# Optimization experiments

Hardware: AMD Instinct MI355X
Metric: run time of the kernel (lower is better)

## Reference

```python
import jax, jax.numpy as jnp
import numpy as np

N = 50000      # nodes
E = 800000     # edges (before self-loops)
F_IN = 128     # node_feature_dim
H = 128        # hidden_dim
HEADS = 4
DH = H // HEADS
L = 3          # num_layers
OUT = 128      # output_dim
B = 64         # graphs in batch
EPS = 1e-5
NEG_SLOPE = 0.2


def layer_norm(x, g, b):
    mu = jnp.mean(x, axis=-1, keepdims=True)
    var = jnp.mean(jnp.square(x - mu), axis=-1, keepdims=True)
    return (x - mu) * jax.lax.rsqrt(var + EPS) * g + b


def setup_inputs() -> dict:
    key = jax.random.key(0)
    ks = jax.random.split(key, 10)
    s = 0.05
    x = jax.random.normal(ks[0], (N, F_IN), jnp.float32)
    edge_index = jax.random.randint(ks[1], (2, E), 0, N, dtype=jnp.int32)
    batch = jnp.sort(jax.random.randint(ks[2], (N,), 0, B, dtype=jnp.int32))
    return {
        "x": x,
        "edge_index": edge_index,
        "batch": batch,
        # node encoder: Linear + LayerNorm
        "W0": jax.random.normal(ks[3], (F_IN, H), jnp.float32) * s,
        "b0": jnp.zeros((H,), jnp.float32),
        "g0": jnp.ones((H,), jnp.float32),
        "be0": jnp.zeros((H,), jnp.float32),
        # GAT layers (stacked over L)
        "Wg": jax.random.normal(ks[4], (L, H, H), jnp.float32) * s,
        "att_src": jax.random.normal(ks[5], (L, HEADS, DH), jnp.float32) * s,
        "att_dst": jax.random.normal(ks[6], (L, HEADS, DH), jnp.float32) * s,
        "bg": jnp.zeros((L, H), jnp.float32),
        "gg": jnp.ones((L, H), jnp.float32),
        "bgg": jnp.zeros((L, H), jnp.float32),
        # output projection: Linear + LayerNorm
        "Wp": jax.random.normal(ks[7], (H, OUT), jnp.float32) * s,
        "bp": jnp.zeros((OUT,), jnp.float32),
        "gp": jnp.ones((OUT,), jnp.float32),
        "bep": jnp.zeros((OUT,), jnp.float32),
    }


def gnn_forward(x, src, dst, W0, b0, g0, be0, Wg, att_src, att_dst, bg, gg, bgg, Wp, bp, gp, bep, batch):
    n = x.shape[0]
    h = jax.nn.silu(layer_norm(x @ W0 + b0, g0, be0))  # [N, H]
    for l in range(L):
        identity = h
        hh = (h @ Wg[l]).reshape(n, HEADS, DH)                 # [N, heads, dh]
        a_s = jnp.einsum('nhd,hd->nh', hh, att_src[l])         # [N, heads]
        a_d = jnp.einsum('nhd,hd->nh', hh, att_dst[l])
        e = jax.nn.leaky_relu(a_s[src] + a_d[dst], NEG_SLOPE)  # [E', heads]
        m = jax.lax.stop_gradient(jax.ops.segment_max(e, dst, num_segments=n))
        alpha = jnp.exp(e - m[dst])
        denom = jax.ops.segment_sum(alpha, dst, num_segments=n)
        alpha = alpha / denom[dst]                             # segment softmax over dst
        msg = hh[src] * alpha[:, :, None]                      # [E', heads, dh]
        out = jax.ops.segment_sum(msg, dst, num_segments=n).reshape(n, H) + bg[l]
        h = jax.nn.silu(layer_norm(out, gg[l], bgg[l])) + identity
    # global mean pool per graph
    cnt = jax.ops.segment_sum(jnp.ones((n, 1), h.dtype), batch, num_segments=B)
    pooled = jax.ops.segment_sum(h, batch, num_segments=B) / jnp.maximum(cnt, 1.0)
    return jax.nn.silu(layer_norm(pooled @ Wp + bp, gp, bep))  # [B, OUT]


def reference(x, edge_index, batch, W0, b0, g0, be0, Wg, att_src, att_dst, bg, gg, bgg, Wp, bp, gp, bep):
    n = x.shape[0]
    loops = jnp.arange(n, dtype=edge_index.dtype)  # PyG GATConv add_self_loops=True
    src = jnp.concatenate([edge_index[0], loops])
    dst = jnp.concatenate([edge_index[1], loops])
    return gnn_forward(x, src, dst, W0, b0, g0, be0, Wg, att_src, att_dst, bg, gg, bgg, Wp, bp, gp, bep, batch)
```

## Files before the change

kernel.cpp:

```cpp
#include <hip/hip_runtime.h>

#define NN    50000
#define EE    800000
#define EPE   850000
#define NPAD  50048
#define BGR   64
#define MAXCH 128
#define NB    98
#define CHUNK 4096
#define NBLK  208
#define BCAP  12288

typedef __attribute__((ext_vector_type(8))) short bf16x8;
typedef __attribute__((ext_vector_type(4))) float f32x4;
typedef __attribute__((ext_vector_type(2))) float f32x2;

__device__ __forceinline__ float bf2f(unsigned short u) {
    return __uint_as_float(((unsigned)u) << 16);
}
__device__ __forceinline__ unsigned short f2bf(float f) {
    unsigned u = __float_as_uint(f);
    unsigned r = (u + 0x7FFFu + ((u >> 16) & 1u)) >> 16;
    return (unsigned short)r;
}
__device__ __forceinline__ float silu(float y) { return y / (1.f + __expf(-y)); }

__global__ void transpose_zero(const float* __restrict__ W0, const float* __restrict__ Wg,
                               unsigned short* __restrict__ WT, float* __restrict__ pooled) {
    __shared__ unsigned short tile[128][129];
    int b = blockIdx.x;
    if (b < 4) {
        const float* src = (b == 0) ? W0 : (Wg + (b - 1) * 16384);
        unsigned short* dst = WT + b * 16384;
        for (int i = threadIdx.x; i < 16384; i += 256) tile[i >> 7][i & 127] = f2bf(src[i]);
        __syncthreads();
        for (int i = threadIdx.x; i < 16384; i += 256) {
            int c = i >> 7, k = i & 127;
            dst[i] = tile[k][c];
        }
    } else {
        int j = (b - 4) * 256 + threadIdx.x;
        if (j < BGR * 128) pooled[j] = 0.f;
    }
}

__global__ __launch_bounds__(256) void bucket_hist(const int* __restrict__ eidx,
                                                   int* __restrict__ hist_blk) {
    __shared__ int lh[NB];
    for (int t = threadIdx.x; t < NB; t += 256) lh[t] = 0;
    __syncthreads();
    int base = blockIdx.x * CHUNK;
#pragma unroll
    for (int j = 0; j < CHUNK / 256; ++j) {
        int i = base + j * 256 + threadIdx.x;
        if (i < EPE) {
            int d = (i < EE) ? eidx[EE + i] : (i - EE);
            atomicAdd(&lh[d >> 9], 1);
        }
    }
    __syncthreads();
    for (int t = threadIdx.x; t < NB; t += 256)
        hist_blk[blockIdx.x * NB + t] = lh[t];
}

__global__ void scan_buckets(const int* __restrict__ hist_blk, int* __restrict__ blkOfs,
                             int* __restrict__ bucketBase) {
    __shared__ int tot[NB];
    __shared__ int base[NB];
    int t = threadIdx.x;
    if (t < NB) {
        int s = 0;
        for (int k = 0; k < NBLK; ++k) s += hist_blk[k * NB + t];
        tot[t] = s;
    }
    __syncthreads();
    if (t == 0) {
        int run = 0;
        for (int b = 0; b < NB; ++b) { base[b] = run; run += tot[b]; }
        bucketBase[NB] = EPE;
    }
    __syncthreads();
    if (t < NB) {
        int run = base[t];
        bucketBase[t] = run;
        for (int k = 0; k < NBLK; ++k) {
            blkOfs[k * NB + t] = run;
            run += hist_blk[k * NB + t];
        }
    }
}

__global__ __launch_bounds__(256) void bin_edges(const int* __restrict__ eidx,
                                                 const int* __restrict__ blkOfs,
                                                 unsigned* __restrict__ binned) {
    __shared__ unsigned staged[CHUNK];
    __shared__ int lhist[NB];
    __shared__ int lscan[NB];
    __shared__ int cnt2[NB];
    __shared__ int gofs[NB];
    int tid = threadIdx.x;
    for (int t = tid; t < NB; t += 256) { lhist[t] = 0; cnt2[t] = 0; }
    __syncthreads();
    int base = blockIdx.x * CHUNK;
    unsigned pk[CHUNK / 256];
#pragma unroll
    for (int j = 0; j < CHUNK / 256; ++j) {
        int i = base + j * 256 + tid;
        pk[j] = 0xFFFFFFFFu;
        if (i < EPE) {
            int s, d;
            if (i < EE) { s = eidx[i]; d = eidx[EE + i]; } else { s = i - EE; d = i - EE; }
            pk[j] = ((unsigned)s << 16) | (unsigned)d;
            atomicAdd(&lhist[d >> 9], 1);
        }
    }
    __syncthreads();
    if (tid == 0) {
        int run = 0;
        for (int b = 0; b < NB; ++b) { lscan[b] = run; run += lhist[b]; }
    }
    __syncthreads();
#pragma unroll
    for (int j = 0; j < CHUNK / 256; ++j) {
        if (pk[j] != 0xFFFFFFFFu) {
            int b = (int)((pk[j] & 0xFFFFu) >> 9);
            int lp = lscan[b] + atomicAdd(&cnt2[b], 1);
            staged[lp] = pk[j];
        }
    }
    for (int t = tid; t < NB; t += 256) gofs[t] = blkOfs[blockIdx.x * NB + t];
    __syncthreads();
    int nTot = lscan[NB - 1] + lhist[NB - 1];
    for (int i = tid; i < nTot; i += 256) {
        unsigned p = staged[i];
        int b = (int)((p & 0xFFFFu) >> 9);
        binned[gofs[b] + (i - lscan[b])] = p;
    }
}

__global__ __launch_bounds__(256) void build_csr(const unsigned* __restrict__ binned,
                                                 const int* __restrict__ bucketBase,
                                                 int* __restrict__ offs,
                                                 int* __restrict__ csr) {
    __shared__ int lcsr[BCAP];
    __shared__ int lcnt[512];
    __shared__ int lofs[512];
    __shared__ int lcur[512];
    __shared__ int psum[256];
    int b = blockIdx.x, tid = threadIdx.x;
    int n0 = b * 512;
    int o0 = bucketBase[b];
    int nTot = bucketBase[b + 1] - o0;
    if (nTot > BCAP) nTot = BCAP;
    for (int j = tid; j < 512; j += 256) lcnt[j] = 0;
    __syncthreads();
    for (int i = tid; i < nTot; i += 256)
        atomicAdd(&lcnt[binned[o0 + i] & 511u], 1);
    __syncthreads();
    int a0 = lcnt[2 * tid], a1 = lcnt[2 * tid + 1];
    psum[tid] = a0 + a1;
    __syncthreads();
    for (int d = 1; d < 256; d <<= 1) {
        int v = (tid >= d) ? psum[tid - d] : 0;
        __syncthreads(); psum[tid] += v; __syncthreads();
    }
    int exclPair = psum[tid] - (a0 + a1);
    lofs[2 * tid] = exclPair;
    lofs[2 * tid + 1] = exclPair + a0;
    lcur[2 * tid] = exclPair;
    lcur[2 * tid + 1] = exclPair + a0;
    __syncthreads();
    for (int j = tid; j < 512; j += 256) {
        int node = n0 + j;
        if (node < NN) offs[node] = o0 + lofs[j];
    }
    if (b == 0 && tid == 0) offs[NN] = EPE;
    for (int i = tid; i < nTot; i += 256) {
        unsigned p = binned[o0 + i];
        int pos = atomicAdd(&lcur[p & 511u], 1);
        if (pos < BCAP) lcsr[pos] = (int)(p >> 16);
    }
    __syncthreads();
    for (int i = tid; i < nTot; i += 256)
        csr[o0 + i] = lcsr[i];
}

__global__ __launch_bounds__(256) void gemm_encoder(
    const float* __restrict__ x, const unsigned short* __restrict__ WT,
    const float* __restrict__ b0, const float* __restrict__ g0,
    const float* __restrict__ be0, unsigned short* __restrict__ h) {
    int wave = threadIdx.x >> 6, lane = threadIdx.x & 63;
    int cl = lane & 15, q = lane >> 4;
    int row0 = blockIdx.x * 64 + wave * 16;
    int rA = row0 + cl; if (rA >= NN) rA = NN - 1;
    int kq = q * 8;
    f32x4 acc[8];
#pragma unroll
    for (int t = 0; t < 8; ++t) acc[t] = (f32x4){0.f, 0.f, 0.f, 0.f};
#pragma unroll
    for (int k0 = 0; k0 < 128; k0 += 32) {
        const float* xr = x + rA * 128 + k0 + kq;
        f32x4 f0 = *(const f32x4*)(xr);
        f32x4 f1 = *(const f32x4*)(xr + 4);
        bf16x8 a;
#pragma unroll
        for (int j = 0; j < 4; ++j) {
            a[j] = (short)f2bf(f0[j]);
            a[4 + j] = (short)f2bf(f1[j]);
        }
#pragma unroll
        for (int t = 0; t < 8; ++t) {
            bf16x8 b = *(const bf16x8*)(WT + (t * 16 + cl) * 128 + k0 + kq);
            acc[t] = __builtin_amdgcn_mfma_f32_16x16x32_bf16(a, b, acc[t], 0, 0, 0);
        }
    }
    float bcol[8], gcol[8], becol[8];
#pragma unroll
    for (int t = 0; t < 8; ++t) {
        int c = t * 16 + cl;
        bcol[t] = b0[c]; gcol[t] = g0[c]; becol[t] = be0[c];
    }
#pragma unroll
    for (int r = 0; r < 4; ++r) {
        int row = row0 + q * 4 + r;
        float v[8], s = 0.f, ss = 0.f;
#pragma unroll
        for (int t = 0; t < 8; ++t) {
            v[t] = acc[t][r] + bcol[t];
            s += v[t]; ss += v[t] * v[t];
        }
#pragma unroll
        for (int m = 1; m <= 8; m <<= 1) {
            s += __shfl_xor(s, m, 64); ss += __shfl_xor(ss, m, 64);
        }
        float mu = s * (1.f / 128.f);
        float var = ss * (1.f / 128.f) - mu * mu;
        float rstd = rsqrtf(var + 1e-5f);
        if (row < NN) {
#pragma unroll
            for (int t = 0; t < 8; ++t) {
                float y = (v[t] - mu) * rstd * gcol[t] + becol[t];
                h[row * 128 + t * 16 + cl] = f2bf(silu(y));
            }
        }
    }
}

__global__ __launch_bounds__(256) void gemm_gat(
    const unsigned short* __restrict__ h, const unsigned short* __restrict__ WT,
    const float* __restrict__ atts, const float* __restrict__ attd,
    unsigned char* __restrict__ hh8, float* __restrict__ a_s, float* __restrict__ a_d,
    float* __restrict__ es) {
    int wave = threadIdx.x >> 6, lane = threadIdx.x & 63;
    int cl = lane & 15, q = lane >> 4;
    int row0 = blockIdx.x * 64 + wave * 16;
    int rA = row0 + cl; if (rA >= NN) rA = NN - 1;
    int kq = q * 8;
    f32x4 acc[8];
#pragma unroll
    for (int t = 0; t < 8; ++t) acc[t] = (f32x4){0.f, 0.f, 0.f, 0.f};
#pragma unroll
    for (int k0 = 0; k0 < 128; k0 += 32) {
        bf16x8 a = *(const bf16x8*)(h + rA * 128 + k0 + kq);
#pragma unroll
        for (int t = 0; t < 8; ++t) {
            bf16x8 b = *(const bf16x8*)(WT + (t * 16 + cl) * 128 + k0 + kq);
            acc[t] = __builtin_amdgcn_mfma_f32_16x16x32_bf16(a, b, acc[t], 0, 0, 0);
        }
    }
#pragma unroll
    for (int r = 0; r < 4; ++r) {
        int row = row0 + q * 4 + r;
        if (row < NN) {
#pragma unroll
            for (int t = 0; t < 8; ++t) {
                unsigned pk = (unsigned)__builtin_amdgcn_cvt_pk_fp8_f32(acc[t][r], acc[t][r], 0, false);
                hh8[row * 128 + t * 16 + cl] = (unsigned char)(pk & 0xFFu);
            }
        }
    }
    float as_lo[4], as_hi[4], ad_lo[4], ad_hi[4];
#pragma unroll
    for (int hd = 0; hd < 4; ++hd) {
        as_lo[hd] = atts[hd * 32 + cl];      as_hi[hd] = atts[hd * 32 + 16 + cl];
        ad_lo[hd] = attd[hd * 32 + cl];      ad_hi[hd] = attd[hd * 32 + 16 + cl];
    }
#pragma unroll
    for (int r = 0; r < 4; ++r) {
        int row = row0 + q * 4 + r;
        float ps[4], pd[4];
#pragma unroll
        for (int hd = 0; hd < 4; ++hd) {
            float v0 = acc[2 * hd][r], v1 = acc[2 * hd + 1][r];
            ps[hd] = v0 * as_lo[hd] + v1 * as_hi[hd];
            pd[hd] = v0 * ad_lo[hd] + v1 * ad_hi[hd];
        }
#pragma unroll
        for (int m = 1; m <= 8; m <<= 1) {
#pragma unroll
            for (int hd = 0; hd < 4; ++hd) {
                ps[hd] += __shfl_xor(ps[hd], m, 64);
                pd[hd] += __shfl_xor(pd[hd], m, 64);
            }
        }
        if (row < NN && cl < 4) {
            float vs = (cl == 0) ? ps[0] : (cl == 1) ? ps[1] : (cl == 2) ? ps[2] : ps[3];
            float vd = (cl == 0) ? pd[0] : (cl == 1) ? pd[1] : (cl == 2) ? pd[2] : pd[3];
            a_s[row * 4 + cl] = vs;
            a_d[row * 4 + cl] = vd;
            float e = vs + vd;
            es[row * 4 + cl] = (e > 0.f) ? e : 0.2f * e;
        }
    }
}

__global__ __launch_bounds__(256) void gat_aggregate(
    const int* __restrict__ offs, const int* __restrict__ csr,
    const float* __restrict__ a_s, const float* __restrict__ a_d,
    const float* __restrict__ es, const unsigned char* __restrict__ hh8,
    unsigned short* __restrict__ h,
    const float* __restrict__ bg, const float* __restrict__ gg,
    const float* __restrict__ bgg) {
    __shared__ f32x4 lw[8][MAXCH];
    int wv = threadIdx.x >> 6;
    int lane = threadIdx.x & 63;
    int half = lane >> 5;
    int l32 = lane & 31;
    int ns = wv * 2 + half;
    int node = blockIdx.x * 8 + ns;
    int e0 = offs[node], e1 = offs[node + 1];
    int c0 = l32 * 4;
    int hd = l32 >> 3;
    f32x4 ad4 = *(const f32x4*)(a_d + node * 4);
    f32x4 e4  = *(const f32x4*)(es  + node * 4);
    float dacc[4];
    f32x4 xacc[4];
#pragma unroll
    for (int u = 0; u < 4; ++u) {
        dacc[u] = 0.f;
        xacc[u] = (f32x4){0.f, 0.f, 0.f, 0.f};
    }
    for (int base = e0; base < e1; base += MAXCH) {
        int cend = min(e1, base + MAXCH);
        for (int e = base + l32; e < cend; e += 32) {
            int s = csr[e];
            f32x4 as = *(const f32x4*)(a_s + s * 4);
            f32x4 o;
#pragma unroll
            for (int k = 0; k < 4; ++k) {
                float qq = as[k] + ad4[k];
                qq = (qq > 0.f) ? qq : 0.2f * qq;
                o[k] = __expf(qq - e4[k]);
            }
            lw[ns][e - base] = o;
        }
        asm volatile("s_waitcnt lgkmcnt(0)" ::: "memory");
        int n = cend - base;
        int j = 0;
        for (; j + 4 <= n; j += 4) {
            int s0 = csr[base + j], s1 = csr[base + j + 1];
            int s2 = csr[base + j + 2], s3 = csr[base + j + 3];
            float w0 = lw[ns][j + 0][hd];
            float w1 = lw[ns][j + 1][hd];
            float w2 = lw[ns][j + 2][hd];
            float w3 = lw[ns][j + 3][hd];
            unsigned v0 = *(const unsigned*)(hh8 + s0 * 128 + c0);
            unsigned v1 = *(const unsigned*)(hh8 + s1 * 128 + c0);
            unsigned v2 = *(const unsigned*)(hh8 + s2 * 128 + c0);
            unsigned v3 = *(const unsigned*)(hh8 + s3 * 128 + c0);
            f32x2 l0 = __builtin_amdgcn_cvt_pk_f32_fp8(v0, false);
            f32x2 h0 = __builtin_amdgcn_cvt_pk_f32_fp8(v0, true);
            f32x2 l1 = __builtin_amdgcn_cvt_pk_f32_fp8(v1, false);
            f32x2 h1 = __builtin_amdgcn_cvt_pk_f32_fp8(v1, true);
            f32x2 l2 = __builtin_amdgcn_cvt_pk_f32_fp8(v2, false);
            f32x2 h2 = __builtin_amdgcn_cvt_pk_f32_fp8(v2, true);
            f32x2 l3 = __builtin_amdgcn_cvt_pk_f32_fp8(v3, false);
            f32x2 h3 = __builtin_amdgcn_cvt_pk_f32_fp8(v3, true);
            dacc[0] += w0;
            xacc[0][0] += w0 * l0[0]; xacc[0][1] += w0 * l0[1];
            xacc[0][2] += w0 * h0[0]; xacc[0][3] += w0 * h0[1];
            dacc[1] += w1;
            xacc[1][0] += w1 * l1[0]; xacc[1][1] += w1 * l1[1];
            xacc[1][2] += w1 * h1[0]; xacc[1][3] += w1 * h1[1];
            dacc[2] += w2;
            xacc[2][0] += w2 * l2[0]; xacc[2][1] += w2 * l2[1];
            xacc[2][2] += w2 * h2[0]; xacc[2][3] += w2 * h2[1];
            dacc[3] += w3;
            xacc[3][0] += w3 * l3[0]; xacc[3][1] += w3 * l3[1];
            xacc[3][2] += w3 * h3[0]; xacc[3][3] += w3 * h3[1];
        }
        for (; j < n; ++j) {
            int s0 = csr[base + j];
            float w0 = lw[ns][j][hd];
            unsigned v0 = *(const unsigned*)(hh8 + s0 * 128 + c0);
            f32x2 l0 = __builtin_amdgcn_cvt_pk_f32_fp8(v0, false);
            f32x2 h0 = __builtin_amdgcn_cvt_pk_f32_fp8(v0, true);
            dacc[0] += w0;
            xacc[0][0] += w0 * l0[0]; xacc[0][1] += w0 * l0[1];
            xacc[0][2] += w0 * h0[0]; xacc[0][3] += w0 * h0[1];
        }
        if (cend < e1)
            asm volatile("s_waitcnt lgkmcnt(0)" ::: "memory");
    }
    float den = (dacc[0] + dacc[1]) + (dacc[2] + dacc[3]);
    f32x4 X;
#pragma unroll
    for (int k = 0; k < 4; ++k)
        X[k] = (xacc[0][k] + xacc[1][k]) + (xacc[2][k] + xacc[3][k]);
    float inv = 1.f / den;
    f32x4 bgv  = *(const f32x4*)(bg + c0);
    f32x4 ggv  = *(const f32x4*)(gg + c0);
    f32x4 bggv = *(const f32x4*)(bgg + c0);
    f32x4 o;
    float s = 0.f, ss = 0.f;
#pragma unroll
    for (int k = 0; k < 4; ++k) {
        o[k] = X[k] * inv + bgv[k];
        s += o[k]; ss += o[k] * o[k];
    }
#pragma unroll
    for (int m = 1; m <= 16; m <<= 1) {
        s += __shfl_xor(s, m, 64); ss += __shfl_xor(ss, m, 64);
    }
    float mu = s * (1.f / 128.f);
    float var = ss * (1.f / 128.f) - mu * mu;
    float rstd = rsqrtf(var + 1e-5f);
    uint2 idpk = *(const uint2*)(h + node * 128 + c0);
    float r0 = silu((o[0] - mu) * rstd * ggv[0] + bggv[0]) + bf2f((unsigned short)(idpk.x & 0xFFFFu));
    float r1 = silu((o[1] - mu) * rstd * ggv[1] + bggv[1]) + bf2f((unsigned short)(idpk.x >> 16));
    float r2 = silu((o[2] - mu) * rstd * ggv[2] + bggv[2]) + bf2f((unsigned short)(idpk.y & 0xFFFFu));
    float r3 = silu((o[3] - mu) * rstd * ggv[3] + bggv[3]) + bf2f((unsigned short)(idpk.y >> 16));
    uint2 pk;
    pk.x = (unsigned)f2bf(r0) | ((unsigned)f2bf(r1) << 16);
    pk.y = (unsigned)f2bf(r2) | ((unsigned)f2bf(r3) << 16);
    *(uint2*)(h + node * 128 + c0) = pk;
}

__global__ void pool_kernel(const unsigned short* __restrict__ h, const int* __restrict__ batch,
                            float* __restrict__ pooled) {
    int c = threadIdx.x;
    int r0 = blockIdx.x * 64;
    int rend = r0 + 64; if (rend > NN) rend = NN;
    int cur = batch[r0];
    float acc = 0.f;
    for (int r = r0; r < rend; ++r) {
        int b = batch[r];
        float v = bf2f(h[r * 128 + c]);
        if (b != cur) {
            atomicAdd(&pooled[cur * 128 + c], acc);
            acc = 0.f; cur = b;
        }
        acc += v;
    }
    atomicAdd(&pooled[cur * 128 + c], acc);
}

__global__ void final_kernel(const float* __restrict__ pooled, const int* __restrict__ batch,
                             const float* __restrict__ Wp, const float* __restrict__ bp,
                             const float* __restrict__ gp, const float* __restrict__ bep,
                             float* __restrict__ out) {
    __shared__ float p[128];
    __shared__ float red[128];
    __shared__ int bounds[2];
    int g = blockIdx.x, c = threadIdx.x;
    if (c == 0) {
        int lo = 0, hi = NN;
        while (lo < hi) { int m = (lo + hi) >> 1; if (batch[m] < g) lo = m + 1; else hi = m; }
        bounds[0] = lo;
        int lo2 = lo, hi2 = NN;
        while (lo2 < hi2) { int m = (lo2 + hi2) >> 1; if (batch[m] < g + 1) lo2 = m + 1; else hi2 = m; }
        bounds[1] = lo2;
    }
    __syncthreads();
    float cnt = (float)(bounds[1] - bounds[0]); if (cnt < 1.f) cnt = 1.f;
    p[c] = pooled[g * 128 + c] / cnt;
    __syncthreads();
    float acc = bp[c];
    for (int k = 0; k < 128; ++k) acc += p[k] * Wp[k * 128 + c];
    red[c] = acc;
    __syncthreads();
    if (c < 64) {
        float s = red[c] + red[c + 64];
#pragma unroll
        for (int m = 1; m <= 32; m <<= 1) s += __shfl_xor(s, m, 64);
        if (c == 0) red[0] = s;
    }
    __syncthreads();
    float mu = red[0] * (1.f / 128.f);
    __syncthreads();
    float dv = acc - mu;
    red[c] = dv * dv;
    __syncthreads();
    if (c < 64) {
        float s = red[c] + red[c + 64];
#pragma unroll
        for (int m = 1; m <= 32; m <<= 1) s += __shfl_xor(s, m, 64);
        if (c == 0) red[0] = s;
    }
    __syncthreads();
    float var = red[0] * (1.f / 128.f);
    float rstd = rsqrtf(var + 1e-5f);
    float y = dv * rstd * gp[c] + bep[c];
    out[g * 128 + c] = silu(y);
}

extern "C" void kernel_launch(void* const* d_in, const int* in_sizes, int n_in,
                              void* d_out, int out_size, void* d_ws, size_t ws_size,
                              hipStream_t stream) {
    const float* x    = (const float*)d_in[0];
    const int*   eidx = (const int*)d_in[1];
    const int*   batch= (const int*)d_in[2];
    const float* W0   = (const float*)d_in[3];
    const float* b0   = (const float*)d_in[4];
    const float* g0   = (const float*)d_in[5];
    const float* be0  = (const float*)d_in[6];
    const float* Wg   = (const float*)d_in[7];
    const float* atts = (const float*)d_in[8];
    const float* attd = (const float*)d_in[9];
    const float* bg   = (const float*)d_in[10];
    const float* gg   = (const float*)d_in[11];
    const float* bgg  = (const float*)d_in[12];
    const float* Wp   = (const float*)d_in[13];
    const float* bp   = (const float*)d_in[14];
    const float* gp   = (const float*)d_in[15];
    const float* bep  = (const float*)d_in[16];

    char* ws = (char*)d_ws;
    size_t off = 0;
    auto alloc = [&](size_t bytes) {
        void* p = ws + off;
        off = (off + bytes + 255) & ~(size_t)255;
        return p;
    };
    unsigned short* h        = (unsigned short*)alloc((size_t)NPAD * 128 * 2);
    unsigned char*  hh8      = (unsigned char*)alloc((size_t)NN * 128);
    float*          a_s      = (float*)alloc((size_t)NN * 4 * 4);
    float*          a_d      = (float*)alloc((size_t)NN * 4 * 4);
    float*          es       = (float*)alloc((size_t)NN * 4 * 4);
    int*            offs     = (int*)alloc((size_t)(NN + 1) * 4);
    int*            csr      = (int*)alloc((size_t)EPE * 4);
    unsigned*       binned   = (unsigned*)alloc((size_t)EPE * 4);
    int*            hist_blk = (int*)alloc((size_t)NBLK * NB * 4);
    int*            blkOfs   = (int*)alloc((size_t)NBLK * NB * 4);
    int*            bktBase  = (int*)alloc((size_t)(NB + 1) * 4);
    unsigned short* WT       = (unsigned short*)alloc(4 * 16384 * 2);
    float*          pooled   = (float*)alloc((size_t)BGR * 128 * 4);

    transpose_zero<<<4 + 32, 256, 0, stream>>>(W0, Wg, WT, pooled);
    bucket_hist<<<NBLK, 256, 0, stream>>>(eidx, hist_blk);
    scan_buckets<<<1, 128, 0, stream>>>(hist_blk, blkOfs, bktBase);
    bin_edges<<<NBLK, 256, 0, stream>>>(eidx, blkOfs, binned);
    build_csr<<<NB, 256, 0, stream>>>(binned, bktBase, offs, csr);

    gemm_encoder<<<NPAD / 64, 256, 0, stream>>>(x, WT, b0, g0, be0, h);
    for (int l = 0; l < 3; ++l) {
        gemm_gat<<<NPAD / 64, 256, 0, stream>>>(h, WT + (l + 1) * 16384,
                                                atts + l * 128, attd + l * 128,
                                                hh8, a_s, a_d, es);
        gat_aggregate<<<NN / 8, 256, 0, stream>>>(offs, csr, a_s, a_d, es, hh8, h,
                                                  bg + l * 128, gg + l * 128,
                                                  bgg + l * 128);
    }
    pool_kernel<<<(NN + 63) / 64, 128, 0, stream>>>(h, batch, pooled);
    final_kernel<<<BGR, 128, 0, stream>>>(pooled, batch, Wp, bp, gp, bep, (float*)d_out);
}
```

Measured before the change: 381.2 us.

## Fuse preprocessing kernels with encoder/GAT GEMMs and relayout fp8 features

Merges the weight transpose, pool zeroing and edge histogram into one launch. The bucket scan rides alongside the encoder GEMM, and edge binning rides alongside the first GAT GEMM, so independent CSR-building work runs concurrently with dense work and fewer kernels launch. The fp8 projected features are stored with a head-interleaved column layout. The aggregation kernel caches both source indices and all four head weights in shared memory, then accumulates per-column across heads, which removes repeated csr reads. This trades simpler, coalesced per-node epilogue writes for scalar bf16 stores and extra shuffles for the denominator.

```diff
diff --git a/kernel.cpp b/kernel.cpp
--- a/kernel.cpp
+++ b/kernel.cpp
@@ -5,11 +5,11 @@
 #define EPE   850000
 #define NPAD  50048
 #define BGR   64
-#define MAXCH 128
 #define NB    98
 #define CHUNK 4096
 #define NBLK  208
 #define BCAP  12288
+#define AGCH  64
 
 typedef __attribute__((ext_vector_type(8))) short bf16x8;
 typedef __attribute__((ext_vector_type(4))) float f32x4;
@@ -25,9 +25,14 @@
 }
 __device__ __forceinline__ float silu(float y) { return y / (1.f + __expf(-y)); }
 
-__global__ void transpose_zero(const float* __restrict__ W0, const float* __restrict__ Wg,
-                               unsigned short* __restrict__ WT, float* __restrict__ pooled) {
+__global__ __launch_bounds__(256) void pre_kernel(const float* __restrict__ W0,
+                                                  const float* __restrict__ Wg,
+                                                  unsigned short* __restrict__ WT,
+                                                  float* __restrict__ pooled,
+                                                  const int* __restrict__ eidx,
+                                                  int* __restrict__ hist_blk) {
     __shared__ unsigned short tile[128][129];
+    __shared__ int lh[NB];
     int b = blockIdx.x;
     if (b < 4) {
         const float* src = (b == 0) ? W0 : (Wg + (b - 1) * 16384);
@@ -38,70 +43,215 @@
             int c = i >> 7, k = i & 127;
             dst[i] = tile[k][c];
         }
+    } else if (b < 36) {
+        int j = (b - 4) * 256 + threadIdx.x;
+        pooled[j] = 0.f;
     } else {
-        int j = (b - 4) * 256 + threadIdx.x;
-        if (j < BGR * 128) pooled[j] = 0.f;
-    }
-}
-
-__global__ __launch_bounds__(256) void bucket_hist(const int* __restrict__ eidx,
-                                                   int* __restrict__ hist_blk) {
-    __shared__ int lh[NB];
-    for (int t = threadIdx.x; t < NB; t += 256) lh[t] = 0;
-    __syncthreads();
-    int base = blockIdx.x * CHUNK;
-#pragma unroll
-    for (int j = 0; j < CHUNK / 256; ++j) {
-        int i = base + j * 256 + threadIdx.x;
-        if (i < EPE) {
-            int d = (i < EE) ? eidx[EE + i] : (i - EE);
-            atomicAdd(&lh[d >> 9], 1);
-        }
-    }
-    __syncthreads();
-    for (int t = threadIdx.x; t < NB; t += 256)
-        hist_blk[blockIdx.x * NB + t] = lh[t];
-}
-
-__global__ void scan_buckets(const int* __restrict__ hist_blk, int* __restrict__ blkOfs,
-                             int* __restrict__ bucketBase) {
+        int cb = b - 36;
+        for (int t = threadIdx.x; t < NB; t += 256) lh[t] = 0;
+        __syncthreads();
+        int base = cb * CHUNK;
+#pragma unroll
+        for (int j = 0; j < CHUNK / 256; ++j) {
+            int i = base + j * 256 + threadIdx.x;
+            if (i < EPE) {
+                int d = (i < EE) ? eidx[EE + i] : (i - EE);
+                atomicAdd(&lh[d >> 9], 1);
+            }
+        }
+        __syncthreads();
+        for (int t = threadIdx.x; t < NB; t += 256)
+            hist_blk[cb * NB + t] = lh[t];
+    }
+}
+
+__global__ __launch_bounds__(256) void scan_encoder_kernel(
+    const int* __restrict__ hist_blk, int* __restrict__ blkOfs, int* __restrict__ bucketBase,
+    const float* __restrict__ x, const unsigned short* __restrict__ WT,
+    const float* __restrict__ b0, const float* __restrict__ g0,
+    const float* __restrict__ be0, unsigned short* __restrict__ h) {
     __shared__ int tot[NB];
-    __shared__ int base[NB];
-    int t = threadIdx.x;
-    if (t < NB) {
-        int s = 0;
-        for (int k = 0; k < NBLK; ++k) s += hist_blk[k * NB + t];
-        tot[t] = s;
-    }
-    __syncthreads();
-    if (t == 0) {
-        int run = 0;
-        for (int b = 0; b < NB; ++b) { base[b] = run; run += tot[b]; }
-        bucketBase[NB] = EPE;
-    }
-    __syncthreads();
-    if (t < NB) {
-        int run = base[t];
-        bucketBase[t] = run;
-        for (int k = 0; k < NBLK; ++k) {
-            blkOfs[k * NB + t] = run;
-            run += hist_blk[k * NB + t];
-        }
-    }
-}
-
-__global__ __launch_bounds__(256) void bin_edges(const int* __restrict__ eidx,
-                                                 const int* __restrict__ blkOfs,
-                                                 unsigned* __restrict__ binned) {
+    __shared__ int bas[NB];
+    if (blockIdx.x == 0) {
+        int t = threadIdx.x;
+        if (t < NB) {
+            int s = 0;
+            for (int k = 0; k < NBLK; ++k) s += hist_blk[k * NB + t];
+            tot[t] = s;
+        }
+        __syncthreads();
+        if (t == 0) {
+            int run = 0;
+            for (int b = 0; b < NB; ++b) { bas[b] = run; run += tot[b]; }
+            bucketBase[NB] = EPE;
+        }
+        __syncthreads();
+        if (t < NB) {
+            int run = bas[t];
+            bucketBase[t] = run;
+            for (int k = 0; k < NBLK; ++k) {
+                blkOfs[k * NB + t] = run;
+                run += hist_blk[k * NB + t];
+            }
+        }
+        return;
+    }
+    int bid = blockIdx.x - 1;
+    int wave = threadIdx.x >> 6, lane = threadIdx.x & 63;
+    int cl = lane & 15, q = lane >> 4;
+    int row0 = bid * 64 + wave * 16;
+    int rA = row0 + cl; if (rA >= NN) rA = NN - 1;
+    int kq = q * 8;
+    f32x4 acc[8];
+#pragma unroll
+    for (int t = 0; t < 8; ++t) acc[t] = (f32x4){0.f, 0.f, 0.f, 0.f};
+#pragma unroll
+    for (int k0 = 0; k0 < 128; k0 += 32) {
+        const float* xr = x + rA * 128 + k0 + kq;
+        f32x4 f0 = *(const f32x4*)(xr);
+        f32x4 f1 = *(const f32x4*)(xr + 4);
+        bf16x8 a;
+#pragma unroll
+        for (int j = 0; j < 4; ++j) {
+            a[j] = (short)f2bf(f0[j]);
+            a[4 + j] = (short)f2bf(f1[j]);
+        }
+#pragma unroll
+        for (int t = 0; t < 8; ++t) {
+            bf16x8 b = *(const bf16x8*)(WT + (t * 16 + cl) * 128 + k0 + kq);
+            acc[t] = __builtin_amdgcn_mfma_f32_16x16x32_bf16(a, b, acc[t], 0, 0, 0);
+        }
+    }
+    float bcol[8], gcol[8], becol[8];
+#pragma unroll
+    for (int t = 0; t < 8; ++t) {
+        int c = t * 16 + cl;
+        bcol[t] = b0[c]; gcol[t] = g0[c]; becol[t] = be0[c];
+    }
+#pragma unroll
+    for (int r = 0; r < 4; ++r) {
+        int row = row0 + q * 4 + r;
+        float v[8], s = 0.f, ss = 0.f;
+#pragma unroll
+        for (int t = 0; t < 8; ++t) {
+            v[t] = acc[t][r] + bcol[t];
+            s += v[t]; ss += v[t] * v[t];
+        }
+#pragma unroll
+        for (int m = 1; m <= 8; m <<= 1) {
+            s += __shfl_xor(s, m, 64); ss += __shfl_xor(ss, m, 64);
+        }
+        float mu = s * (1.f / 128.f);
+        float var = ss * (1.f / 128.f) - mu * mu;
+        float rstd = rsqrtf(var + 1e-5f);
+        if (row < NN) {
+#pragma unroll
+            for (int t = 0; t < 8; ++t) {
+                float y = (v[t] - mu) * rstd * gcol[t] + becol[t];
+                h[row * 128 + t * 16 + cl] = f2bf(silu(y));
+            }
+        }
+    }
+}
+
+__device__ __forceinline__ void gat_gemm_body(
+    int bid, const unsigned short* __restrict__ h, const unsigned short* __restrict__ WT,
+    const float* __restrict__ atts, const float* __restrict__ attd,
+    unsigned char* __restrict__ hh8, float* __restrict__ a_s, float* __restrict__ a_d,
+    float* __restrict__ es) {
+    int wave = threadIdx.x >> 6, lane = threadIdx.x & 63;
+    int cl = lane & 15, q = lane >> 4;
+    int row0 = bid * 64 + wave * 16;
+    int rA = row0 + cl; if (rA >= NN) rA = NN - 1;
+    int kq = q * 8;
+    f32x4 acc[8];
+#pragma unroll
+    for (int t = 0; t < 8; ++t) acc[t] = (f32x4){0.f, 0.f, 0.f, 0.f};
+#pragma unroll
+    for (int k0 = 0; k0 < 128; k0 += 32) {
+        bf16x8 a = *(const bf16x8*)(h + rA * 128 + k0 + kq);
+#pragma unroll
+        for (int t = 0; t < 8; ++t) {
+            bf16x8 b = *(const bf16x8*)(WT + (t * 16 + cl) * 128 + k0 + kq);
+            acc[t] = __builtin_amdgcn_mfma_f32_16x16x32_bf16(a, b, acc[t], 0, 0, 0);
+        }
+    }
+#pragma unroll
+    for (int r = 0; r < 4; ++r) {
+        int row = row0 + q * 4 + r;
+        if (row < NN) {
+#pragma unroll
+            for (int t = 0; t < 8; ++t) {
+                unsigned pk = (unsigned)__builtin_amdgcn_cvt_pk_fp8_f32(acc[t][r], acc[t][r], 0, false);
+                int c = t * 16 + cl;
+                hh8[row * 128 + ((c & 31) << 2) + (c >> 5)] = (unsigned char)(pk & 0xFFu);
+            }
+        }
+    }
+    float as_lo[4], as_hi[4], ad_lo[4], ad_hi[4];
+#pragma unroll
+    for (int hd = 0; hd < 4; ++hd) {
+        as_lo[hd] = atts[hd * 32 + cl];      as_hi[hd] = atts[hd * 32 + 16 + cl];
+        ad_lo[hd] = attd[hd * 32 + cl];      ad_hi[hd] = attd[hd * 32 + 16 + cl];
+    }
+#pragma unroll
+    for (int r = 0; r < 4; ++r) {
+        int row = row0 + q * 4 + r;
+        float ps[4], pd[4];
+#pragma unroll
+        for (int hd = 0; hd < 4; ++hd) {
+            float v0 = acc[2 * hd][r], v1 = acc[2 * hd + 1][r];
+            ps[hd] = v0 * as_lo[hd] + v1 * as_hi[hd];
+            pd[hd] = v0 * ad_lo[hd] + v1 * ad_hi[hd];
+        }
+#pragma unroll
+        for (int m = 1; m <= 8; m <<= 1) {
+#pragma unroll
+            for (int hd = 0; hd < 4; ++hd) {
+                ps[hd] += __shfl_xor(ps[hd], m, 64);
+                pd[hd] += __shfl_xor(pd[hd], m, 64);
+            }
+        }
+        if (row < NN && cl < 4) {
+            float vs = (cl == 0) ? ps[0] : (cl == 1) ? ps[1] : (cl == 2) ? ps[2] : ps[3];
+            float vd = (cl == 0) ? pd[0] : (cl == 1) ? pd[1] : (cl == 2) ? pd[2] : pd[3];
+            a_s[row * 4 + cl] = vs;
+            a_d[row * 4 + cl] = vd;
+            float e = vs + vd;
+            es[row * 4 + cl] = (e > 0.f) ? e : 0.2f * e;
+        }
+    }
+}
+
+__global__ __launch_bounds__(256) void gemm_gat(
+    const unsigned short* __restrict__ h, const unsigned short* __restrict__ WT,
+    const float* __restrict__ atts, const float* __restrict__ attd,
+    unsigned char* __restrict__ hh8, float* __restrict__ a_s, float* __restrict__ a_d,
+    float* __restrict__ es) {
+    gat_gemm_body(blockIdx.x, h, WT, atts, attd, hh8, a_s, a_d, es);
+}
+
+__global__ __launch_bounds__(256) void bin_gat_kernel(
+    const int* __restrict__ eidx, const int* __restrict__ blkOfs,
+    unsigned* __restrict__ binned,
+    const unsigned short* __restrict__ h, const unsigned short* __restrict__ WT1,
+    const float* __restrict__ atts, const float* __restrict__ attd,
+    unsigned char* __restrict__ hh8, float* __restrict__ a_s, float* __restrict__ a_d,
+    float* __restrict__ es) {
     __shared__ unsigned staged[CHUNK];
     __shared__ int lhist[NB];
     __shared__ int lscan[NB];
     __shared__ int cnt2[NB];
     __shared__ int gofs[NB];
+    if (blockIdx.x >= NBLK) {
+        gat_gemm_body(blockIdx.x - NBLK, h, WT1, atts, attd, hh8, a_s, a_d, es);
+        return;
+    }
+    int cb = blockIdx.x;
     int tid = threadIdx.x;
     for (int t = tid; t < NB; t += 256) { lhist[t] = 0; cnt2[t] = 0; }
     __syncthreads();
-    int base = blockIdx.x * CHUNK;
+    int base = cb * CHUNK;
     unsigned pk[CHUNK / 256];
 #pragma unroll
     for (int j = 0; j < CHUNK / 256; ++j) {
@@ -128,7 +278,7 @@
             staged[lp] = pk[j];
         }
     }
-    for (int t = tid; t < NB; t += 256) gofs[t] = blkOfs[blockIdx.x * NB + t];
+    for (int t = tid; t < NB; t += 256) gofs[t] = blkOfs[cb * NB + t];
     __syncthreads();
     int nTot = lscan[NB - 1] + lhist[NB - 1];
     for (int i = tid; i < nTot; i += 256) {
@@ -185,135 +335,6 @@
         csr[o0 + i] = lcsr[i];
 }
 
-__global__ __launch_bounds__(256) void gemm_encoder(
-    const float* __restrict__ x, const unsigned short* __restrict__ WT,
-    const float* __restrict__ b0, const float* __restrict__ g0,
-    const float* __restrict__ be0, unsigned short* __restrict__ h) {
-    int wave = threadIdx.x >> 6, lane = threadIdx.x & 63;
-    int cl = lane & 15, q = lane >> 4;
-    int row0 = blockIdx.x * 64 + wave * 16;
-    int rA = row0 + cl; if (rA >= NN) rA = NN - 1;
-    int kq = q * 8;
-    f32x4 acc[8];
-#pragma unroll
-    for (int t = 0; t < 8; ++t) acc[t] = (f32x4){0.f, 0.f, 0.f, 0.f};
-#pragma unroll
-    for (int k0 = 0; k0 < 128; k0 += 32) {
-        const float* xr = x + rA * 128 + k0 + kq;
-        f32x4 f0 = *(const f32x4*)(xr);
-        f32x4 f1 = *(const f32x4*)(xr + 4);
-        bf16x8 a;
-#pragma unroll
-        for (int j = 0; j < 4; ++j) {
-            a[j] = (short)f2bf(f0[j]);
-            a[4 + j] = (short)f2bf(f1[j]);
-        }
-#pragma unroll
-        for (int t = 0; t < 8; ++t) {
-            bf16x8 b = *(const bf16x8*)(WT + (t * 16 + cl) * 128 + k0 + kq);
-            acc[t] = __builtin_amdgcn_mfma_f32_16x16x32_bf16(a, b, acc[t], 0, 0, 0);
-        }
-    }
-    float bcol[8], gcol[8], becol[8];
-#pragma unroll
-    for (int t = 0; t < 8; ++t) {
-        int c = t * 16 + cl;
-        bcol[t] = b0[c]; gcol[t] = g0[c]; becol[t] = be0[c];
-    }
-#pragma unroll
-    for (int r = 0; r < 4; ++r) {
-        int row = row0 + q * 4 + r;
-        float v[8], s = 0.f, ss = 0.f;
-#pragma unroll
-        for (int t = 0; t < 8; ++t) {
-            v[t] = acc[t][r] + bcol[t];
-            s += v[t]; ss += v[t] * v[t];
-        }
-#pragma unroll
-        for (int m = 1; m <= 8; m <<= 1) {
-            s += __shfl_xor(s, m, 64); ss += __shfl_xor(ss, m, 64);
-        }
-        float mu = s * (1.f / 128.f);
-        float var = ss * (1.f / 128.f) - mu * mu;
-        float rstd = rsqrtf(var + 1e-5f);
-        if (row < NN) {
-#pragma unroll
-            for (int t = 0; t < 8; ++t) {
-                float y = (v[t] - mu) * rstd * gcol[t] + becol[t];
-                h[row * 128 + t * 16 + cl] = f2bf(silu(y));
-            }
-        }
-    }
-}
-
-__global__ __launch_bounds__(256) void gemm_gat(
-    const unsigned short* __restrict__ h, const unsigned short* __restrict__ WT,
-    const float* __restrict__ atts, const float* __restrict__ attd,
-    unsigned char* __restrict__ hh8, float* __restrict__ a_s, float* __restrict__ a_d,
-    float* __restrict__ es) {
-    int wave = threadIdx.x >> 6, lane = threadIdx.x & 63;
-    int cl = lane & 15, q = lane >> 4;
-    int row0 = blockIdx.x * 64 + wave * 16;
-    int rA = row0 + cl; if (rA >= NN) rA = NN - 1;
-    int kq = q * 8;
-    f32x4 acc[8];
-#pragma unroll
-    for (int t = 0; t < 8; ++t) acc[t] = (f32x4){0.f, 0.f, 0.f, 0.f};
-#pragma unroll
-    for (int k0 = 0; k0 < 128; k0 += 32) {
-        bf16x8 a = *(const bf16x8*)(h + rA * 128 + k0 + kq);
-#pragma unroll
-        for (int t = 0; t < 8; ++t) {
-            bf16x8 b = *(const bf16x8*)(WT + (t * 16 + cl) * 128 + k0 + kq);
-            acc[t] = __builtin_amdgcn_mfma_f32_16x16x32_bf16(a, b, acc[t], 0, 0, 0);
-        }
-    }
-#pragma unroll
-    for (int r = 0; r < 4; ++r) {
-        int row = row0 + q * 4 + r;
-        if (row < NN) {
-#pragma unroll
-            for (int t = 0; t < 8; ++t) {
-                unsigned pk = (unsigned)__builtin_amdgcn_cvt_pk_fp8_f32(acc[t][r], acc[t][r], 0, false);
-                hh8[row * 128 + t * 16 + cl] = (unsigned char)(pk & 0xFFu);
-            }
-        }
-    }
-    float as_lo[4], as_hi[4], ad_lo[4], ad_hi[4];
-#pragma unroll
-    for (int hd = 0; hd < 4; ++hd) {
-        as_lo[hd] = atts[hd * 32 + cl];      as_hi[hd] = atts[hd * 32 + 16 + cl];
-        ad_lo[hd] = attd[hd * 32 + cl];      ad_hi[hd] = attd[hd * 32 + 16 + cl];
-    }
-#pragma unroll
-    for (int r = 0; r < 4; ++r) {
-        int row = row0 + q * 4 + r;
-        float ps[4], pd[4];
-#pragma unroll
-        for (int hd = 0; hd < 4; ++hd) {
-            float v0 = acc[2 * hd][r], v1 = acc[2 * hd + 1][r];
-            ps[hd] = v0 * as_lo[hd] + v1 * as_hi[hd];
-            pd[hd] = v0 * ad_lo[hd] + v1 * ad_hi[hd];
-        }
-#pragma unroll
-        for (int m = 1; m <= 8; m <<= 1) {
-#pragma unroll
-            for (int hd = 0; hd < 4; ++hd) {
-                ps[hd] += __shfl_xor(ps[hd], m, 64);
-                pd[hd] += __shfl_xor(pd[hd], m, 64);
-            }
-        }
-        if (row < NN && cl < 4) {
-            float vs = (cl == 0) ? ps[0] : (cl == 1) ? ps[1] : (cl == 2) ? ps[2] : ps[3];
-            float vd = (cl == 0) ? pd[0] : (cl == 1) ? pd[1] : (cl == 2) ? pd[2] : pd[3];
-            a_s[row * 4 + cl] = vs;
-            a_d[row * 4 + cl] = vd;
-            float e = vs + vd;
-            es[row * 4 + cl] = (e > 0.f) ? e : 0.2f * e;
-        }
-    }
-}
-
 __global__ __launch_bounds__(256) void gat_aggregate(
     const int* __restrict__ offs, const int* __restrict__ csr,
     const float* __restrict__ a_s, const float* __restrict__ a_d,
@@ -321,7 +342,8 @@
     unsigned short* __restrict__ h,
     const float* __restrict__ bg, const float* __restrict__ gg,
     const float* __restrict__ bgg) {
-    __shared__ f32x4 lw[8][MAXCH];
+    __shared__ int   lss[8][AGCH];
+    __shared__ f32x4 lww[8][AGCH];
     int wv = threadIdx.x >> 6;
     int lane = threadIdx.x & 63;
     int half = lane >> 5;
@@ -329,93 +351,78 @@
     int ns = wv * 2 + half;
     int node = blockIdx.x * 8 + ns;
     int e0 = offs[node], e1 = offs[node + 1];
-    int c0 = l32 * 4;
-    int hd = l32 >> 3;
     f32x4 ad4 = *(const f32x4*)(a_d + node * 4);
     f32x4 e4  = *(const f32x4*)(es  + node * 4);
-    float dacc[4];
-    f32x4 xacc[4];
-#pragma unroll
-    for (int u = 0; u < 4; ++u) {
-        dacc[u] = 0.f;
-        xacc[u] = (f32x4){0.f, 0.f, 0.f, 0.f};
-    }
-    for (int base = e0; base < e1; base += MAXCH) {
-        int cend = min(e1, base + MAXCH);
+    f32x4 dacc = (f32x4){0.f, 0.f, 0.f, 0.f};
+    f32x4 xacc = (f32x4){0.f, 0.f, 0.f, 0.f};
+    const unsigned char* hp = hh8 + l32 * 4;
+    for (int base = e0; base < e1; base += AGCH) {
+        int cend = min(e1, base + AGCH);
+        int n = cend - base;
         for (int e = base + l32; e < cend; e += 32) {
             int s = csr[e];
             f32x4 as = *(const f32x4*)(a_s + s * 4);
-            f32x4 o;
+            f32x4 w;
 #pragma unroll
             for (int k = 0; k < 4; ++k) {
                 float qq = as[k] + ad4[k];
                 qq = (qq > 0.f) ? qq : 0.2f * qq;
-                o[k] = __expf(qq - e4[k]);
+                w[k] = __expf(qq - e4[k]);
+                dacc[k] += w[k];
             }
-            lw[ns][e - base] = o;
+            lss[ns][e - base] = s;
+            lww[ns][e - base] = w;
         }
         asm volatile("s_waitcnt lgkmcnt(0)" ::: "memory");
-        int n = cend - base;
         int j = 0;
         for (; j + 4 <= n; j += 4) {
-            int s0 = csr[base + j], s1 = csr[base + j + 1];
-            int s2 = csr[base + j + 2], s3 = csr[base + j + 3];
-            float w0 = lw[ns][j + 0][hd];
-            float w1 = lw[ns][j + 1][hd];
-            float w2 = lw[ns][j + 2][hd];
-            float w3 = lw[ns][j + 3][hd];
-            unsigned v0 = *(const unsigned*)(hh8 + s0 * 128 + c0);
-            unsigned v1 = *(const unsigned*)(hh8 + s1 * 128 + c0);
-            unsigned v2 = *(const unsigned*)(hh8 + s2 * 128 + c0);
-            unsigned v3 = *(const unsigned*)(hh8 + s3 * 128 + c0);
-            f32x2 l0 = __builtin_amdgcn_cvt_pk_f32_fp8(v0, false);
-            f32x2 h0 = __builtin_amdgcn_cvt_pk_f32_fp8(v0, true);
-            f32x2 l1 = __builtin_amdgcn_cvt_pk_f32_fp8(v1, false);
-            f32x2 h1 = __builtin_amdgcn_cvt_pk_f32_fp8(v1, true);
-            f32x2 l2 = __builtin_amdgcn_cvt_pk_f32_fp8(v2, false);
-            f32x2 h2 = __builtin_amdgcn_cvt_pk_f32_fp8(v2, true);
-            f32x2 l3 = __builtin_amdgcn_cvt_pk_f32_fp8(v3, false);
-            f32x2 h3 = __builtin_amdgcn_cvt_pk_f32_fp8(v3, true);
-            dacc[0] += w0;
-            xacc[0][0] += w0 * l0[0]; xacc[0][1] += w0 * l0[1];
-            xacc[0][2] += w0 * h0[0]; xacc[0][3] += w0 * h0[1];
-            dacc[1] += w1;
-            xacc[1][0] += w1 * l1[0]; xacc[1][1] += w1 * l1[1];
-            xacc[1][2] += w1 * h1[0]; xacc[1][3] += w1 * h1[1];
-            dacc[2] += w2;
-            xacc[2][0] += w2 * l2[0]; xacc[2][1] += w2 * l2[1];
-            xacc[2][2] += w2 * h2[0]; xacc[2][3] += w2 * h2[1];
-            dacc[3] += w3;
-            xacc[3][0] += w3 * l3[0]; xacc[3][1] += w3 * l3[1];
-            xacc[3][2] += w3 * h3[0]; xacc[3][3] += w3 * h3[1];
+            int s0 = lss[ns][j],     s1 = lss[ns][j + 1];
+            int s2 = lss[ns][j + 2], s3 = lss[ns][j + 3];
+            f32x4 w0 = lww[ns][j],     w1 = lww[ns][j + 1];
+            f32x4 w2 = lww[ns][j + 2], w3 = lww[ns][j + 3];
+            unsigned v0 = *(const unsigned*)(hp + ((long)s0 << 7));
+            unsigned v1 = *(const unsigned*)(hp + ((long)s1 << 7));
+            unsigned v2 = *(const unsigned*)(hp + ((long)s2 << 7));
+            unsigned v3 = *(const unsigned*)(hp + ((long)s3 << 7));
+            f32x2 lo0 = __builtin_amdgcn_cvt_pk_f32_fp8(v0, false);
+            f32x2 hi0 = __builtin_amdgcn_cvt_pk_f32_fp8(v0, true);
+            f32x2 lo1 = __builtin_amdgcn_cvt_pk_f32_fp8(v1, false);
+            f32x2 hi1 = __builtin_amdgcn_cvt_pk_f32_fp8(v1, true);
+            f32x2 lo2 = __builtin_amdgcn_cvt_pk_f32_fp8(v2, false);
+            f32x2 hi2 = __builtin_amdgcn_cvt_pk_f32_fp8(v2, true);
+            f32x2 lo3 = __builtin_amdgcn_cvt_pk_f32_fp8(v3, false);
+            f32x2 hi3 = __builtin_amdgcn_cvt_pk_f32_fp8(v3, true);
+            xacc[0] += w0[0] * lo0[0]; xacc[1] += w0[1] * lo0[1];
+            xacc[2] += w0[2] * hi0[0]; xacc[3] += w0[3] * hi0[1];
+            xacc[0] += w1[0] * lo1[0]; xacc[1] += w1[1] * lo1[1];
+            xacc[2] += w1[2] * hi1[0]; xacc[3] += w1[3] * hi1[1];
+            xacc[0] += w2[0] * lo2[0]; xacc[1] += w2[1] * lo2[1];
+            xacc[2] += w2[2] * hi2[0]; xacc[3] += w2[3] * hi2[1];
+            xacc[0] += w3[0] * lo3[0]; xacc[1] += w3[1] * lo3[1];
+            xacc[2] += w3[2] * hi3[0]; xacc[3] += w3[3] * hi3[1];
         }
         for (; j < n; ++j) {
-            int s0 = csr[base + j];
-            float w0 = lw[ns][j][hd];
-            unsigned v0 = *(const unsigned*)(hh8 + s0 * 128 + c0);
-            f32x2 l0 = __builtin_amdgcn_cvt_pk_f32_fp8(v0, false);
-            f32x2 h0 = __builtin_amdgcn_cvt_pk_f32_fp8(v0, true);
-            dacc[0] += w0;
-            xacc[0][0] += w0 * l0[0]; xacc[0][1] += w0 * l0[1];
-            xacc[0][2] += w0 * h0[0]; xacc[0][3] += w0 * h0[1];
+            int s0 = lss[ns][j];
+            f32x4 w0 = lww[ns][j];
+            unsigned v0 = *(const unsigned*)(hp + ((long)s0 << 7));
+            f32x2 lo0 = __builtin_amdgcn_cvt_pk_f32_fp8(v0, false);
+            f32x2 hi0 = __builtin_amdgcn_cvt_pk_f32_fp8(v0, true);
+            xacc[0] += w0[0] * lo0[0]; xacc[1] += w0[1] * lo0[1];
+            xacc[2] += w0[2] * hi0[0]; xacc[3] += w0[3] * hi0[1];
         }
         if (cend < e1)
             asm volatile("s_waitcnt lgkmcnt(0)" ::: "memory");
     }
-    float den = (dacc[0] + dacc[1]) + (dacc[2] + dacc[3]);
-    f32x4 X;
-#pragma unroll
-    for (int k = 0; k < 4; ++k)
-        X[k] = (xacc[0][k] + xacc[1][k]) + (xacc[2][k] + xacc[3][k]);
-    float inv = 1.f / den;
-    f32x4 bgv  = *(const f32x4*)(bg + c0);
-    f32x4 ggv  = *(const f32x4*)(gg + c0);
-    f32x4 bggv = *(const f32x4*)(bgg + c0);
-    f32x4 o;
-    float s = 0.f, ss = 0.f;
+#pragma unroll
+    for (int m = 1; m <= 16; m <<= 1) {
+#pragma unroll
+        for (int k = 0; k < 4; ++k) dacc[k] += __shfl_xor(dacc[k], m, 64);
+    }
+    float o[4], s = 0.f, ss = 0.f;
 #pragma unroll
     for (int k = 0; k < 4; ++k) {
-        o[k] = X[k] * inv + bgv[k];
+        int c = k * 32 + l32;
+        o[k] = xacc[k] / dacc[k] + bg[c];
         s += o[k]; ss += o[k] * o[k];
     }
 #pragma unroll
@@ -425,15 +432,13 @@
     float mu = s * (1.f / 128.f);
     float var = ss * (1.f / 128.f) - mu * mu;
     float rstd = rsqrtf(var + 1e-5f);
-    uint2 idpk = *(const uint2*)(h + node * 128 + c0);
-    float r0 = silu((o[0] - mu) * rstd * ggv[0] + bggv[0]) + bf2f((unsigned short)(idpk.x & 0xFFFFu));
-    float r1 = silu((o[1] - mu) * rstd * ggv[1] + bggv[1]) + bf2f((unsigned short)(idpk.x >> 16));
-    float r2 = silu((o[2] - mu) * rstd * ggv[2] + bggv[2]) + bf2f((unsigned short)(idpk.y & 0xFFFFu));
-    float r3 = silu((o[3] - mu) * rstd * ggv[3] + bggv[3]) + bf2f((unsigned short)(idpk.y >> 16));
-    uint2 pk;
-    pk.x = (unsigned)f2bf(r0) | ((unsigned)f2bf(r1) << 16);
-    pk.y = (unsigned)f2bf(r2) | ((unsigned)f2bf(r3) << 16);
-    *(uint2*)(h + node * 128 + c0) = pk;
+#pragma unroll
+    for (int k = 0; k < 4; ++k) {
+        int c = k * 32 + l32;
+        float y = (o[k] - mu) * rstd * gg[c] + bgg[c];
+        float r = silu(y) + bf2f(h[node * 128 + c]);
+        h[node * 128 + c] = f2bf(r);
+    }
 }
 
 __global__ void pool_kernel(const unsigned short* __restrict__ h, const int* __restrict__ batch,
@@ -546,14 +551,17 @@
     unsigned short* WT       = (unsigned short*)alloc(4 * 16384 * 2);
     float*          pooled   = (float*)alloc((size_t)BGR * 128 * 4);
 
-    transpose_zero<<<4 + 32, 256, 0, stream>>>(W0, Wg, WT, pooled);
-    bucket_hist<<<NBLK, 256, 0, stream>>>(eidx, hist_blk);
-    scan_buckets<<<1, 128, 0, stream>>>(hist_blk, blkOfs, bktBase);
-    bin_edges<<<NBLK, 256, 0, stream>>>(eidx, blkOfs, binned);
+    pre_kernel<<<4 + 32 + NBLK, 256, 0, stream>>>(W0, Wg, WT, pooled, eidx, hist_blk);
+    scan_encoder_kernel<<<1 + NPAD / 64, 256, 0, stream>>>(hist_blk, blkOfs, bktBase,
+                                                           x, WT, b0, g0, be0, h);
+    bin_gat_kernel<<<NBLK + NPAD / 64, 256, 0, stream>>>(eidx, blkOfs, binned,
+                                                         h, WT + 16384, atts, attd,
+                                                         hh8, a_s, a_d, es);
     build_csr<<<NB, 256, 0, stream>>>(binned, bktBase, offs, csr);
 
-    gemm_encoder<<<NPAD / 64, 256, 0, stream>>>(x, WT, b0, g0, be0, h);
-    for (int l = 0; l < 3; ++l) {
+    gat_aggregate<<<NN / 8, 256, 0, stream>>>(offs, csr, a_s, a_d, es, hh8, h,
+                                              bg, gg, bgg);
+    for (int l = 1; l < 3; ++l) {
         gemm_gat<<<NPAD / 64, 256, 0, stream>>>(h, WT + (l + 1) * 16384,
                                                 atts + l * 128, attd + l * 128,
                                                 hh8, a_s, a_d, es);
```

After: 333.5 us. -12.5%, faster.
